# Performance work log

Hardware: AMD Instinct MI355X
Metric: run time of the kernel (lower is better)

Reference implementation:

```python
import jax, jax.numpy as jnp
import numpy as np

LOG2PI = float(np.log(2.0 * np.pi))
MIN_DURATION = 1
NUM_STATES = 512
OBS_DIM = 128
B, T, K = 64, 2000, 400


def setup_inputs() -> dict:
    key = jax.random.key(0)
    ks = jax.random.split(key, 10)
    observations = jax.random.normal(ks[0], (B, T, OBS_DIM), dtype=jnp.float32)
    state_sequence = jax.random.randint(ks[1], (B, K), 0, NUM_STATES, dtype=jnp.int32)
    # durations >= min_duration so gamma log-prob stays finite
    duration_sequence = jax.random.randint(ks[2], (B, K), 1, 51, dtype=jnp.int32)
    # learned parameters, initialized as in the torch module
    alpha_params = jnp.ones((NUM_STATES,), jnp.float32)
    beta_params = jnp.ones((NUM_STATES,), jnp.float32)
    transition_logits = jax.random.normal(ks[3], (NUM_STATES, NUM_STATES), dtype=jnp.float32)
    initial_logits = jnp.zeros((NUM_STATES,), jnp.float32)
    observation_means = jax.random.normal(ks[4], (NUM_STATES, OBS_DIM), dtype=jnp.float32)
    observation_logvars = jnp.zeros((NUM_STATES, OBS_DIM), jnp.float32)
    return {
        "observations": observations,
        "alpha_params": alpha_params,
        "beta_params": beta_params,
        "transition_logits": transition_logits,
        "initial_logits": initial_logits,
        "observation_means": observation_means,
        "observation_logvars": observation_logvars,
        "state_sequence": state_sequence,
        "duration_sequence": duration_sequence,
    }


def _gamma_duration_logprob(alpha_params, beta_params, state_sequence, duration_sequence):
    # fully vectorized version of the per-sample Python loop in DurationModel
    d = duration_sequence.astype(jnp.float32)                      # [B, K]
    alpha = jax.nn.softplus(alpha_params)[state_sequence] + 1e-6   # [B, K]
    beta = jax.nn.softplus(beta_params)[state_sequence] + 1e-6
    lp = (alpha - 1.0) * jnp.log(d + 1e-8) - beta * d
    lp = lp - (jax.lax.lgamma(alpha) - alpha * jnp.log(beta))
    return jnp.where(d >= MIN_DURATION, lp, -jnp.inf)


def reference(observations, alpha_params, beta_params, transition_logits,
              initial_logits, observation_means, observation_logvars,
              state_sequence, duration_sequence):
    # --- duration log-probs per segment: [B, K]
    log_dur = _gamma_duration_logprob(alpha_params, beta_params,
                                      state_sequence, duration_sequence)

    # --- expand segments to frames: frame t belongs to segment with cum[idx-1] <= t < cum[idx]
    cum = jnp.cumsum(duration_sequence, axis=1)                    # [B, K]
    t = jnp.arange(observations.shape[1])                          # [T]
    seg_idx = jax.vmap(lambda c: jnp.searchsorted(c, t, side='right'))(cum)
    seg_idx = jnp.clip(seg_idx, 0, state_sequence.shape[1] - 1)    # [B, T]
    frame_states = jnp.take_along_axis(state_sequence, seg_idx, axis=1)  # [B, T]

    # --- diagonal-gaussian observation log-probs per frame: [B, T]
    mu = observation_means[frame_states]                           # [B, T, D]
    lv = observation_logvars[frame_states]                         # [B, T, D]
    resid2 = (observations - mu) ** 2 * jnp.exp(-lv)
    log_obs = -0.5 * jnp.sum(lv + resid2 + LOG2PI, axis=-1)        # [B, T]

    # --- initial + transition log-probs over the segment-level state chain
    log_trans = jax.nn.log_softmax(transition_logits, axis=-1)     # [S, S]
    log_init = jax.nn.log_softmax(initial_logits)                  # [S]
    trans_lp = log_trans[state_sequence[:, :-1], state_sequence[:, 1:]].sum(axis=1)  # [B]
    init_lp = log_init[state_sequence[:, 0]]                       # [B]

    # --- per-sequence supervised log-likelihood: [B]
    log_likelihood = log_obs.sum(axis=1) + log_dur.sum(axis=1) + trans_lp + init_lp
    return log_likelihood
```

## Files before the change

kernel.cpp:

```cpp
#include <hip/hip_runtime.h>
#include <hip/hip_bf16.h>
#include <math.h>

#define NS 512
#define OD 128
#define BB 64
#define TT 2000
#define KK 400
#define CHUNK 128
#define NCH 16
#define LOG2PI_F 1.8378770664093453f
#define SEQ_OFF  576
#define PART_OFF 1024


__device__ __forceinline__ float softplusf(float x) {
    return (x > 20.f) ? x : log1pf(expf(x));
}

__device__ __forceinline__ float gammlnf(float x) {
    float tmp = x + 5.5f;
    tmp -= (x + 0.5f) * __logf(tmp);
    const float ser = 1.000000000190015f
        + 76.18009172947146f    / (x + 1.f)
        - 86.50532032941677f    / (x + 2.f)
        + 24.01409824083091f    / (x + 3.f)
        - 1.231739572450155f    / (x + 4.f)
        + 1.208650973866179e-3f / (x + 5.f)
        - 5.395239384953e-6f    / (x + 6.f);
    return -tmp + __logf(2.5066282746310005f * ser / x);
}

__global__ __launch_bounds__(512, 8) void big_kernel(
    const float* __restrict__ obs, const float* __restrict__ mu,
    const float* __restrict__ lvar, const float* __restrict__ trans,
    const float* __restrict__ init_logits,
    const float* __restrict__ alpha_p, const float* __restrict__ beta_p,
    const int* __restrict__ states, const int* __restrict__ durs,
    float* __restrict__ ws)
{
    const int tid = threadIdx.x;
    const int bid = blockIdx.x;
    __shared__ float red[8];

    if (bid < BB * NCH) {
        const int b = bid >> 4;
        const int t0 = (bid & 15) * CHUNK;

        __shared__ int fsl[CHUNK];
        __shared__ int csum[8];

        const int lane = tid & 63, w = tid >> 6;
        int sv = 0, dv = 0;
        if (tid < KK) { sv = states[b * KK + tid]; dv = durs[b * KK + tid]; }
        int v = dv;
        #pragma unroll
        for (int off = 1; off < 64; off <<= 1) {
            int u = __shfl_up(v, off, 64);
            if (lane >= off) v += u;
        }
        if (lane == 63) csum[w] = v;
        __syncthreads();
        int woff = 0;
        #pragma unroll
        for (int c = 0; c < 8; ++c) woff += (c < w) ? csum[c] : 0;
        const int cum = v + woff;

        if (tid < KK) {
            int a = cum - dv;
            int e = (tid == KK - 1) ? t0 + CHUNK : cum;
            a = (a < t0) ? t0 : a;
            e = (e > t0 + CHUNK) ? t0 + CHUNK : e;
            for (int t = a; t < e; ++t) fsl[t - t0] = sv;
        }
        __syncthreads();

        const int row = tid >> 5;
        const int dd = (tid & 31) * 4;
        float acc = 0.f;
        if (t0 + CHUNK <= TT) {
            #pragma unroll
            for (int i = 0; i < CHUNK / 16; ++i) {
                const int t = t0 + i * 16 + row;
                const int s = fsl[i * 16 + row];
                const float4 o  = *(const float4*)(obs + ((size_t)(b * TT + t)) * OD + dd);
                const float4 m  = *(const float4*)(mu  + (size_t)s * OD + dd);
                const float4 lv = *(const float4*)(lvar + (size_t)s * OD + dd);
                const float dx = o.x - m.x, dy = o.y - m.y, dz = o.z - m.z, dw = o.w - m.w;
                acc += lv.x + lv.y + lv.z + lv.w + 4.f * LOG2PI_F
                     + dx * dx * __expf(-lv.x) + dy * dy * __expf(-lv.y)
                     + dz * dz * __expf(-lv.z) + dw * dw * __expf(-lv.w);
            }
        } else {
            #pragma unroll
            for (int i = 0; i < CHUNK / 16; ++i) {
                const int t = t0 + i * 16 + row;
                if (t < TT) {
                    const int s = fsl[i * 16 + row];
                    const float4 o  = *(const float4*)(obs + ((size_t)(b * TT + t)) * OD + dd);
                    const float4 m  = *(const float4*)(mu  + (size_t)s * OD + dd);
                    const float4 lv = *(const float4*)(lvar + (size_t)s * OD + dd);
                    const float dx = o.x - m.x, dy = o.y - m.y, dz = o.z - m.z, dw = o.w - m.w;
                    acc += lv.x + lv.y + lv.z + lv.w + 4.f * LOG2PI_F
                         + dx * dx * __expf(-lv.x) + dy * dy * __expf(-lv.y)
                         + dz * dz * __expf(-lv.z) + dw * dw * __expf(-lv.w);
                }
            }
        }
        for (int off = 32; off; off >>= 1) acc += __shfl_down(acc, off, 64);
        if ((tid & 63) == 0) red[tid >> 6] = acc;
        __syncthreads();
        if (tid == 0) {
            float s = 0.f;
            #pragma unroll
            for (int c = 0; c < 8; ++c) s += red[c];
            ws[PART_OFF + bid] = -0.5f * s;
        }
    } else if (bid < BB * NCH + NS + 1) {
        const int r = bid - BB * NCH;
        const float* src = (r < NS) ? (trans + (size_t)r * NS) : init_logits;
        const float x = src[tid];
        float m = x;
        for (int off = 32; off; off >>= 1) m = fmaxf(m, __shfl_down(m, off, 64));
        if ((tid & 63) == 0) red[tid >> 6] = m;
        __syncthreads();
        m = red[0];
        #pragma unroll
        for (int c = 1; c < 8; ++c) m = fmaxf(m, red[c]);
        __syncthreads();
        float e = __expf(x - m);
        for (int off = 32; off; off >>= 1) e += __shfl_down(e, off, 64);
        if ((tid & 63) == 0) red[tid >> 6] = e;
        __syncthreads();
        if (tid == 0) {
            float s = 0.f;
            #pragma unroll
            for (int c = 0; c < 8; ++c) s += red[c];
            ws[(r < NS) ? r : 512] = m + __logf(s);
        }
    } else {
        const int b = bid - (BB * NCH + NS + 1);
        float lp = 0.f;
        if (tid < KK) {
            const int s = states[b * KK + tid];
            const float dvf = (float)durs[b * KK + tid];
            const float a  = softplusf(alpha_p[s]) + 1e-6f;
            const float bt = softplusf(beta_p[s]) + 1e-6f;
            float vv = (a - 1.f) * __logf(dvf + 1e-8f) - bt * dvf
                     + a * __logf(bt) - gammlnf(a);
            lp = (dvf >= 1.f) ? vv : -INFINITY;
            if (tid < KK - 1)
                lp += trans[(size_t)s * NS + states[b * KK + tid + 1]];
        }
        for (int off = 32; off; off >>= 1) lp += __shfl_down(lp, off, 64);
        if ((tid & 63) == 0) red[tid >> 6] = lp;
        __syncthreads();
        if (tid == 0) {
            float s = 0.f;
            #pragma unroll
            for (int c = 0; c < 8; ++c) s += red[c];
            ws[SEQ_OFF + b] = s + init_logits[states[b * KK]];
        }
    }
}

__global__ __launch_bounds__(256) void fin_kernel(
    const int* __restrict__ states, const float* __restrict__ ws,
    float* __restrict__ out)
{
    const int b = blockIdx.x;
    const int tid = threadIdx.x;
    __shared__ float red[4];

    float lp = 0.f;
    if (tid < NCH)       lp = ws[PART_OFF + b * NCH + tid];
    else if (tid == NCH) lp = ws[SEQ_OFF + b] - ws[512];
    for (int k = tid; k < KK - 1; k += 256)
        lp -= ws[states[b * KK + k]];
    for (int off = 32; off; off >>= 1) lp += __shfl_down(lp, off, 64);
    if ((tid & 63) == 0) red[tid >> 6] = lp;
    __syncthreads();
    if (tid == 0)
        out[b] = red[0] + red[1] + red[2] + red[3];
}

extern "C" void kernel_launch(void* const* d_in, const int* in_sizes, int n_in,
                              void* d_out, int out_size, void* d_ws, size_t ws_size,
                              hipStream_t stream) {
    const float* observations = (const float*)d_in[0];
    const float* alpha_p      = (const float*)d_in[1];
    const float* beta_p       = (const float*)d_in[2];
    const float* trans        = (const float*)d_in[3];
    const float* init_logits  = (const float*)d_in[4];
    const float* obs_means    = (const float*)d_in[5];
    const float* obs_logvars  = (const float*)d_in[6];
    const int*   state_seq    = (const int*)d_in[7];
    const int*   dur_seq      = (const int*)d_in[8];

    float* ws = (float*)d_ws;
    float* out = (float*)d_out;

    big_kernel<<<BB * NCH + NS + 1 + BB, 512, 0, stream>>>(
        observations, obs_means, obs_logvars, trans, init_logits,
        alpha_p, beta_p, state_seq, dur_seq, ws);
    fin_kernel<<<BB, 256, 0, stream>>>(state_seq, ws, out);
}
```

Baseline: 22.41 us.

## Fuse finalize into main kernel via atomics and per-block transition normalizers

Removes the separate finalize kernel and the 513 per-row log-softmax blocks. Each of the 64 per-sequence blocks now recomputes all 512 transition-row exp-sums in shared memory, applies the log normalizer inline, and atomically adds its result into the output. The observation chunks also atomically add their partials, and a memset zeroes the output first. This trades a kernel launch and workspace round-trip for redundant reading of the transition matrix in every sequence block. It also drops the max-subtraction in the softmax, which risks overflow for large logits.

```diff
diff --git a/kernel.cpp b/kernel.cpp
--- a/kernel.cpp
+++ b/kernel.cpp
@@ -10,9 +10,6 @@
 #define CHUNK 128
 #define NCH 16
 #define LOG2PI_F 1.8378770664093453f
-#define SEQ_OFF  576
-#define PART_OFF 1024
-
 
 __device__ __forceinline__ float softplusf(float x) {
     return (x > 20.f) ? x : log1pf(expf(x));
@@ -37,10 +34,11 @@
     const float* __restrict__ init_logits,
     const float* __restrict__ alpha_p, const float* __restrict__ beta_p,
     const int* __restrict__ states, const int* __restrict__ durs,
-    float* __restrict__ ws)
+    float* __restrict__ out)
 {
     const int tid = threadIdx.x;
     const int bid = blockIdx.x;
+    const int lane = tid & 63, w = tid >> 6;
     __shared__ float red[8];
 
     if (bid < BB * NCH) {
@@ -50,7 +48,6 @@
         __shared__ int fsl[CHUNK];
         __shared__ int csum[8];
 
-        const int lane = tid & 63, w = tid >> 6;
         int sv = 0, dv = 0;
         if (tid < KK) { sv = states[b * KK + tid]; dv = durs[b * KK + tid]; }
         int v = dv;
@@ -114,32 +111,33 @@
             float s = 0.f;
             #pragma unroll
             for (int c = 0; c < 8; ++c) s += red[c];
-            ws[PART_OFF + bid] = -0.5f * s;
+            atomicAdd(out + b, -0.5f * s);
         }
-    } else if (bid < BB * NCH + NS + 1) {
-        const int r = bid - BB * NCH;
-        const float* src = (r < NS) ? (trans + (size_t)r * NS) : init_logits;
-        const float x = src[tid];
-        float m = x;
-        for (int off = 32; off; off >>= 1) m = fmaxf(m, __shfl_down(m, off, 64));
-        if ((tid & 63) == 0) red[tid >> 6] = m;
-        __syncthreads();
-        m = red[0];
-        #pragma unroll
-        for (int c = 1; c < 8; ++c) m = fmaxf(m, red[c]);
-        __syncthreads();
-        float e = __expf(x - m);
-        for (int off = 32; off; off >>= 1) e += __shfl_down(e, off, 64);
-        if ((tid & 63) == 0) red[tid >> 6] = e;
+    } else {
+        const int b = bid - BB * NCH;
+        __shared__ float S[NS];
+        __shared__ float init_lse;
+
+        for (int r = w; r < NS; r += 8) {
+            float sum = 0.f;
+            #pragma unroll
+            for (int c = 0; c < 8; ++c)
+                sum += __expf(trans[(size_t)r * NS + c * 64 + lane]);
+            for (int off = 32; off; off >>= 1) sum += __shfl_down(sum, off, 64);
+            if (lane == 0) S[r] = sum;
+        }
+        float ei = __expf(init_logits[tid]);
+        for (int off = 32; off; off >>= 1) ei += __shfl_down(ei, off, 64);
+        if (lane == 0) red[w] = ei;
         __syncthreads();
         if (tid == 0) {
-            float s = 0.f;
+            float t = 0.f;
             #pragma unroll
-            for (int c = 0; c < 8; ++c) s += red[c];
-            ws[(r < NS) ? r : 512] = m + __logf(s);
+            for (int c = 0; c < 8; ++c) t += red[c];
+            init_lse = __logf(t);
         }
-    } else {
-        const int b = bid - (BB * NCH + NS + 1);
+        __syncthreads();
+
         float lp = 0.f;
         if (tid < KK) {
             const int s = states[b * KK + tid];
@@ -150,7 +148,8 @@
                      + a * __logf(bt) - gammlnf(a);
             lp = (dvf >= 1.f) ? vv : -INFINITY;
             if (tid < KK - 1)
-                lp += trans[(size_t)s * NS + states[b * KK + tid + 1]];
+                lp += trans[(size_t)s * NS + states[b * KK + tid + 1]]
+                    - __logf(S[s]);
         }
         for (int off = 32; off; off >>= 1) lp += __shfl_down(lp, off, 64);
         if ((tid & 63) == 0) red[tid >> 6] = lp;
@@ -159,29 +158,9 @@
             float s = 0.f;
             #pragma unroll
             for (int c = 0; c < 8; ++c) s += red[c];
-            ws[SEQ_OFF + b] = s + init_logits[states[b * KK]];
+            atomicAdd(out + b, s + init_logits[states[b * KK]] - init_lse);
         }
     }
-}
-
-__global__ __launch_bounds__(256) void fin_kernel(
-    const int* __restrict__ states, const float* __restrict__ ws,
-    float* __restrict__ out)
-{
-    const int b = blockIdx.x;
-    const int tid = threadIdx.x;
-    __shared__ float red[4];
-
-    float lp = 0.f;
-    if (tid < NCH)       lp = ws[PART_OFF + b * NCH + tid];
-    else if (tid == NCH) lp = ws[SEQ_OFF + b] - ws[512];
-    for (int k = tid; k < KK - 1; k += 256)
-        lp -= ws[states[b * KK + k]];
-    for (int off = 32; off; off >>= 1) lp += __shfl_down(lp, off, 64);
-    if ((tid & 63) == 0) red[tid >> 6] = lp;
-    __syncthreads();
-    if (tid == 0)
-        out[b] = red[0] + red[1] + red[2] + red[3];
 }
 
 extern "C" void kernel_launch(void* const* d_in, const int* in_sizes, int n_in,
@@ -197,11 +176,10 @@
     const int*   state_seq    = (const int*)d_in[7];
     const int*   dur_seq      = (const int*)d_in[8];
 
-    float* ws = (float*)d_ws;
     float* out = (float*)d_out;
 
-    big_kernel<<<BB * NCH + NS + 1 + BB, 512, 0, stream>>>(
+    hipMemsetAsync(out, 0, BB * sizeof(float), stream);
+    big_kernel<<<BB * NCH + BB, 512, 0, stream>>>(
         observations, obs_means, obs_logvars, trans, init_logits,
-        alpha_p, beta_p, state_seq, dur_seq, ws);
-    fin_kernel<<<BB, 256, 0, stream>>>(state_seq, ws, out);
+        alpha_p, beta_p, state_seq, dur_seq, out);
 }
```

After: 60.50 us. 2.7x slower.
